# Kernel tuning notes

Hardware: AMD Instinct MI355X
Metric: run time of the kernel (lower is better)

## Reference

```python
import jax, jax.numpy as jnp
import numpy as np
from jax import lax

N = 4096      # nodes
D = 256       # in_channels
H = 128       # hidden_size (cell output = 2*H = 256)
BLOCK = 128   # row-block size for the masked-max scan
THR = 0.99    # adjacency threshold on uniform A -> avg degree ~41
EPS = 1e-12


def _block_max(m, scores):
    # m: [BLOCK, N] bool, scores: [N, H] -> [BLOCK, H]
    v = jnp.where(m[:, :, None], scores[None, :, :], -jnp.inf)
    return v.max(axis=1)

_block_max = jax.checkpoint(_block_max)


def masked_max(mask, scores):
    # maxpool over neighbors, blocked over destination nodes to avoid an [N,N,H] temp
    n = mask.shape[0]
    mblk = mask.reshape(n // BLOCK, BLOCK, n)
    def body(_, m):
        return None, _block_max(m, scores)
    _, out = lax.scan(body, None, mblk)
    out = out.reshape(n, scores.shape[-1])
    # nodes with no neighbors -> 0
    return jnp.where(jnp.isneginf(out), jnp.zeros_like(out), out)


def setup_inputs() -> dict:
    key = jax.random.key(0)
    ks = jax.random.split(key, 16)
    def w(k, shape):
        fan = shape[0]
        return (jax.random.normal(k, shape, jnp.float32) / np.sqrt(fan)).astype(jnp.float32)
    D1 = 2 * H  # layer-1 input dim (= 256)
    return dict(
        x=jax.random.normal(ks[0], (N, D), jnp.float32),
        A=jax.random.uniform(ks[1], (N, N), dtype=jnp.float32),
        # layer 0 cell params
        Wp0=w(ks[2], (D, H)), bp0=jnp.zeros((H,), jnp.float32),
        Ws0=w(ks[3], (D, H)), bs0=jnp.zeros((H,), jnp.float32),
        Wn0=w(ks[4], (H, H)), bn0=jnp.zeros((H,), jnp.float32),
        # layer 1 cell params
        Wp1=w(ks[5], (D1, H)), bp1=jnp.zeros((H,), jnp.float32),
        Ws1=w(ks[6], (D1, H)), bs1=jnp.zeros((H,), jnp.float32),
        Wn1=w(ks[7], (H, H)), bn1=jnp.zeros((H,), jnp.float32),
    )


def _cell(x, mask, Wp, bp, Ws, bs, Wn, bn):
    # GraphSAGE maxpool cell: concat(self transform, neighbor maxpool transform)
    scores = jax.nn.relu(x @ Wp + bp)                 # [N, H]
    pooled = masked_max(mask, scores)                 # [N, H]
    return jnp.concatenate([x @ Ws + bs, pooled @ Wn + bn], axis=-1)  # [N, 2H]


def reference(x, A, Wp0, bp0, Ws0, bs0, Wn0, bn0, Wp1, bp1, Ws1, bs1, Wn1, bn1):
    mask = A > THR  # [N, N] bool adjacency
    for (Wp, bp, Ws, bs, Wn, bn) in ((Wp0, bp0, Ws0, bs0, Wn0, bn0),
                                     (Wp1, bp1, Ws1, bs1, Wn1, bn1)):
        x = _cell(x, mask, Wp, bp, Ws, bs, Wn, bn)
        x = jax.nn.relu(x)
        nrm = jnp.linalg.norm(x, axis=-1, keepdims=True)
        x = x / jnp.maximum(nrm, EPS)
    return x
```

## Files before the change

kernel.cpp:

```cpp
#include <hip/hip_runtime.h>

#define NN 4096
#define CAP 256
#define THRV 0.99f

typedef __attribute__((ext_vector_type(8))) short short8v;
typedef __attribute__((ext_vector_type(4))) float f32x4;

__device__ inline unsigned short f2bf(float f) {
  unsigned u = __builtin_bit_cast(unsigned, f);
  u = (u + 0x7fffu + ((u >> 16) & 1u)) >> 16;
  return (unsigned short)u;
}
__device__ inline unsigned pkmax(unsigned a, unsigned b) {
  unsigned r;
  asm("v_pk_max_u16 %0, %1, %2" : "=v"(r) : "v"(a), "v"(b));
  return r;
}
__device__ inline uint4 max4(uint4 a, uint4 b) {
  return make_uint4(pkmax(a.x, b.x), pkmax(a.y, b.y), pkmax(a.z, b.z), pkmax(a.w, b.w));
}


__global__ __launch_bounds__(256) void kA(
    const float* __restrict__ x, const float* __restrict__ A,
    const float* __restrict__ Wp0, const float* __restrict__ bp0,
    const float* __restrict__ Ws0, const float* __restrict__ bs0,
    const float* __restrict__ Wn0, const float* __restrict__ Wp1,
    const float* __restrict__ Ws1, const float* __restrict__ Wn1,
    int* __restrict__ cnt, unsigned short* __restrict__ nbr,
    unsigned short* __restrict__ scores0, float* __restrict__ S0,
    unsigned short* __restrict__ tWn0, unsigned short* __restrict__ tWp1,
    unsigned short* __restrict__ tWs1, unsigned short* __restrict__ tWn1) {
  const int bid = blockIdx.x;
  if (bid < NN) {
    int row = bid;
    __shared__ int sc;
    __shared__ unsigned short sn[CAP];
    if (threadIdx.x == 0) sc = 0;
    __syncthreads();
    const float4* Arow = (const float4*)(A + (size_t)row * NN);
#pragma unroll
    for (int it = 0; it < 4; ++it) {
      int j4 = it * 256 + threadIdx.x;
      float4 v = Arow[j4];
      int j = j4 * 4;
      if (v.x > THRV) { int p = atomicAdd(&sc, 1); if (p < CAP) sn[p] = (unsigned short)(j); }
      if (v.y > THRV) { int p = atomicAdd(&sc, 1); if (p < CAP) sn[p] = (unsigned short)(j + 1); }
      if (v.z > THRV) { int p = atomicAdd(&sc, 1); if (p < CAP) sn[p] = (unsigned short)(j + 2); }
      if (v.w > THRV) { int p = atomicAdd(&sc, 1); if (p < CAP) sn[p] = (unsigned short)(j + 3); }
    }
    __syncthreads();
    int c = min(sc, CAP);
    if (threadIdx.x == 0) cnt[row] = c;
    for (int k = threadIdx.x; k < c; k += 256) nbr[(size_t)row * CAP + k] = sn[k];
    return;
  }
  if (bid < NN + 128) {
    const int wv = threadIdx.x >> 6, lane = threadIdx.x & 63;
    const int unit = (bid - NN) * 4 + wv;
    const int set = unit >> 8;
    const int rb = unit & 255;
    const float* W = set ? Ws0 : Wp0;
    const float* bias = set ? bs0 : bp0;
    const int g = lane >> 4, r15 = lane & 15;
    const int row = rb * 16 + r15;
    f32x4 acc[8] = {};
    for (int kt = 0; kt < 256; kt += 32) {
      const float* xp = x + (size_t)row * 256 + kt + 4 * g;
      float4 lo = *(const float4*)xp;
      float4 hi = *(const float4*)(xp + 16);
      short8v a;
      a[0] = (short)f2bf(lo.x); a[1] = (short)f2bf(lo.y);
      a[2] = (short)f2bf(lo.z); a[3] = (short)f2bf(lo.w);
      a[4] = (short)f2bf(hi.x); a[5] = (short)f2bf(hi.y);
      a[6] = (short)f2bf(hi.z); a[7] = (short)f2bf(hi.w);
#pragma unroll
      for (int nf = 0; nf < 8; ++nf) {
        const float* wp = W + (size_t)(kt + 4 * g) * 128 + nf * 16 + r15;
        short8v b;
#pragma unroll
        for (int j = 0; j < 4; ++j) b[j] = (short)f2bf(wp[(size_t)j * 128]);
#pragma unroll
        for (int j = 0; j < 4; ++j) b[4 + j] = (short)f2bf(wp[(size_t)(16 + j) * 128]);
        acc[nf] = __builtin_amdgcn_mfma_f32_16x16x32_bf16(a, b, acc[nf], 0, 0, 0);
      }
    }
#pragma unroll
    for (int nf = 0; nf < 8; ++nf) {
      int col = nf * 16 + r15;
      float bv = bias[col];
#pragma unroll
      for (int r = 0; r < 4; ++r) {
        int orow = rb * 16 + 4 * g + r;
        float t = acc[nf][r] + bv;
        if (set == 0) scores0[(size_t)orow * 128 + col] = f2bf(fmaxf(t, 0.f));
        else          S0[(size_t)orow * 128 + col] = t;
      }
    }
    return;
  }
  int id = bid - NN - 128;
  const float* src; unsigned short* dst; int base;
  if (id < 16)      { src = Wn0; dst = tWn0; base = id; }
  else if (id < 48) { src = Wp1; dst = tWp1; base = id - 16; }
  else if (id < 80) { src = Ws1; dst = tWs1; base = id - 48; }
  else              { src = Wn1; dst = tWn1; base = id - 80; }
  int e0 = base * 1024 + threadIdx.x * 4;
  float4 v = *(const float4*)(src + e0);
  int k = e0 >> 7, n = e0 & 127;
  float vv[4] = {v.x, v.y, v.z, v.w};
  int elem = (k & 3) + 4 * ((k >> 4) & 1);
  int gg = (k >> 2) & 3;
  int fragkt = (k >> 5) * 8;
#pragma unroll
  for (int i = 0; i < 4; ++i) {
    int nn = n + i;
    int idx = ((fragkt + (nn >> 4)) << 9) + ((gg * 16 + (nn & 15)) << 3) + elem;
    dst[idx] = f2bf(vv[i]);
  }
}

template<int LAYER>
__global__ __launch_bounds__(512) void fusedL(
    const int* __restrict__ cnt, const unsigned short* __restrict__ nbr,
    const unsigned short* __restrict__ scores_in, const float* __restrict__ S_in,
    const unsigned short* __restrict__ tWn, const float* __restrict__ bn,
    const unsigned short* __restrict__ tWp, const float* __restrict__ bp,
    const unsigned short* __restrict__ tWs, const float* __restrict__ bs,
    unsigned short* __restrict__ scores_out, float* __restrict__ S_out,
    float* __restrict__ out) {
  __shared__ int scnt[16];
  __shared__ unsigned short snb[16][CAP];
  __shared__ unsigned short pool2[16][2][136];
  __shared__ unsigned short pooled[16][136];
  __shared__ unsigned short xb[16][264];
  __shared__ float ssqs[16];
  __shared__ float ssqw[4][16];

  const int tid = threadIdx.x;
  const int wv = tid >> 6, lane = tid & 63, g = lane >> 4, r15 = lane & 15;
  const int r0 = blockIdx.x * 16;

  if (tid < 16) scnt[tid] = cnt[r0 + tid];
  {
    const ushort4* src = (const ushort4*)(nbr + (size_t)r0 * CAP);
    ushort4* dst = (ushort4*)snb;
    dst[tid] = src[tid];
    dst[tid + 512] = src[tid + 512];
  }
  __syncthreads();

  {
    const int r = tid >> 5, sub = tid & 31;
    const int h = sub >> 4, c8 = (sub & 15) * 8;
    const int c = scnt[r];
    uint4 m0 = make_uint4(0, 0, 0, 0), m1 = m0, m2 = m0, m3 = m0;
    int k = h;
    for (; k + 6 < c; k += 8) {
      int j0 = snb[r][k], j1 = snb[r][k + 2], j2 = snb[r][k + 4], j3 = snb[r][k + 6];
      uint4 a0 = *(const uint4*)(scores_in + (size_t)j0 * 128 + c8);
      uint4 a1 = *(const uint4*)(scores_in + (size_t)j1 * 128 + c8);
      uint4 a2 = *(const uint4*)(scores_in + (size_t)j2 * 128 + c8);
      uint4 a3 = *(const uint4*)(scores_in + (size_t)j3 * 128 + c8);
      m0 = max4(m0, a0); m1 = max4(m1, a1); m2 = max4(m2, a2); m3 = max4(m3, a3);
    }
    for (; k < c; k += 2)
      m0 = max4(m0, *(const uint4*)(scores_in + (size_t)snb[r][k] * 128 + c8));
    *(uint4*)&pool2[r][h][c8] = max4(max4(m0, m1), max4(m2, m3));
  }
  __syncthreads();
  if (tid < 256) {
    const int r = tid >> 4, c8 = (tid & 15) * 8;
    uint4 a = *(const uint4*)&pool2[r][0][c8];
    uint4 b = *(const uint4*)&pool2[r][1][c8];
    *(uint4*)&pooled[r][c8] = max4(a, b);
  }
  __syncthreads();

  float sv[8];
  f32x4 pacc[2] = {};
  const int srow = tid >> 4, sc8 = (tid & 15) * 8;
  if (tid < 256) {
    const float* sp = S_in + (size_t)(r0 + srow) * 128 + sc8;
    float4 sa = *(const float4*)sp;
    float4 sb = *(const float4*)(sp + 4);
    sv[0] = fmaxf(sa.x, 0.f); sv[1] = fmaxf(sa.y, 0.f);
    sv[2] = fmaxf(sa.z, 0.f); sv[3] = fmaxf(sa.w, 0.f);
    sv[4] = fmaxf(sb.x, 0.f); sv[5] = fmaxf(sb.y, 0.f);
    sv[6] = fmaxf(sb.z, 0.f); sv[7] = fmaxf(sb.w, 0.f);
    float ps = 0.f;
#pragma unroll
    for (int i = 0; i < 8; ++i) ps += sv[i] * sv[i];
#pragma unroll
    for (int off = 1; off < 16; off <<= 1) ps += __shfl_xor(ps, off, 16);
    if ((tid & 15) == 0) ssqs[srow] = ps;
  } else {
    const int wv2 = wv - 4;
#pragma unroll
    for (int kt = 0; kt < 128; kt += 32) {
      ushort4 alo = *(const ushort4*)&pooled[r15][kt + 4 * g];
      ushort4 ahi = *(const ushort4*)&pooled[r15][kt + 16 + 4 * g];
      short8v a;
      a[0] = alo.x; a[1] = alo.y; a[2] = alo.z; a[3] = alo.w;
      a[4] = ahi.x; a[5] = ahi.y; a[6] = ahi.z; a[7] = ahi.w;
#pragma unroll
      for (int f = 0; f < 2; ++f) {
        uint4 bw = *((const uint4*)(tWn + (size_t)((kt >> 5) * 8 + 2 * wv2 + f) * 512) + lane);
        pacc[f] = __builtin_amdgcn_mfma_f32_16x16x32_bf16(a, __builtin_bit_cast(short8v, bw), pacc[f], 0, 0, 0);
      }
    }
#pragma unroll
    for (int f = 0; f < 2; ++f) {
      float bv = bn[(2 * wv2 + f) * 16 + r15];
#pragma unroll
      for (int rr = 0; rr < 4; ++rr) pacc[f][rr] = fmaxf(pacc[f][rr] + bv, 0.f);
    }
#pragma unroll
    for (int rr = 0; rr < 4; ++rr) {
      float ps = pacc[0][rr] * pacc[0][rr] + pacc[1][rr] * pacc[1][rr];
#pragma unroll
      for (int off = 1; off < 16; off <<= 1) ps += __shfl_xor(ps, off, 16);
      if (r15 == 0) ssqw[wv2][4 * g + rr] = ps;
    }
  }
  __syncthreads();

  if (LAYER == 0) {
    if (tid < 256) {
      float tot = ssqs[srow] + ssqw[0][srow] + ssqw[1][srow] + ssqw[2][srow] + ssqw[3][srow];
      float sc = 1.f / fmaxf(sqrtf(tot), 1e-12f);
      unsigned short hh[8];
#pragma unroll
      for (int i = 0; i < 8; ++i) hh[i] = f2bf(sv[i] * sc);
      uint4 wvv;
      wvv.x = (unsigned)hh[0] | ((unsigned)hh[1] << 16);
      wvv.y = (unsigned)hh[2] | ((unsigned)hh[3] << 16);
      wvv.z = (unsigned)hh[4] | ((unsigned)hh[5] << 16);
      wvv.w = (unsigned)hh[6] | ((unsigned)hh[7] << 16);
      *(uint4*)&xb[srow][sc8] = wvv;
    } else {
      const int wv2 = wv - 4;
#pragma unroll
      for (int rr = 0; rr < 4; ++rr) {
        int row = 4 * g + rr;
        float tot = ssqs[row] + ssqw[0][row] + ssqw[1][row] + ssqw[2][row] + ssqw[3][row];
        float sc = 1.f / fmaxf(sqrtf(tot), 1e-12f);
#pragma unroll
        for (int f = 0; f < 2; ++f)
          xb[row][128 + (2 * wv2 + f) * 16 + r15] = f2bf(pacc[f][rr] * sc);
      }
    }
    __syncthreads();
    const int s = wv >> 2;
    const unsigned short* Wt = s ? tWs : tWp;
    const float* bb = s ? bs : bp;
    const int nf0 = (wv & 3) * 2;
    f32x4 dacc[2] = {};
#pragma unroll
    for (int kt = 0; kt < 256; kt += 32) {
      ushort4 alo = *(const ushort4*)&xb[r15][kt + 4 * g];
      ushort4 ahi = *(const ushort4*)&xb[r15][kt + 16 + 4 * g];
      short8v a;
      a[0] = alo.x; a[1] = alo.y; a[2] = alo.z; a[3] = alo.w;
      a[4] = ahi.x; a[5] = ahi.y; a[6] = ahi.z; a[7] = ahi.w;
#pragma unroll
      for (int f = 0; f < 2; ++f) {
        uint4 bw = *((const uint4*)(Wt + (size_t)((kt >> 5) * 8 + nf0 + f) * 512) + lane);
        dacc[f] = __builtin_amdgcn_mfma_f32_16x16x32_bf16(a, __builtin_bit_cast(short8v, bw), dacc[f], 0, 0, 0);
      }
    }
#pragma unroll
    for (int f = 0; f < 2; ++f) {
      int col = (nf0 + f) * 16 + r15;
      float bv = bb[col];
#pragma unroll
      for (int rr = 0; rr < 4; ++rr) {
        int grow = r0 + 4 * g + rr;
        float t = dacc[f][rr] + bv;
        if (s == 0) scores_out[(size_t)grow * 128 + col] = f2bf(fmaxf(t, 0.f));
        else        S_out[(size_t)grow * 128 + col] = t;
      }
    }
  } else {
    if (tid < 256) {
      float tot = ssqs[srow] + ssqw[0][srow] + ssqw[1][srow] + ssqw[2][srow] + ssqw[3][srow];
      float sc = 1.f / fmaxf(sqrtf(tot), 1e-12f);
      float* op = out + (size_t)(r0 + srow) * 256 + sc8;
      *(float4*)op = make_float4(sv[0] * sc, sv[1] * sc, sv[2] * sc, sv[3] * sc);
      *(float4*)(op + 4) = make_float4(sv[4] * sc, sv[5] * sc, sv[6] * sc, sv[7] * sc);
    } else {
      const int wv2 = wv - 4;
#pragma unroll
      for (int rr = 0; rr < 4; ++rr) {
        int row = 4 * g + rr;
        float tot = ssqs[row] + ssqw[0][row] + ssqw[1][row] + ssqw[2][row] + ssqw[3][row];
        float sc = 1.f / fmaxf(sqrtf(tot), 1e-12f);
#pragma unroll
        for (int f = 0; f < 2; ++f)
          out[(size_t)(r0 + row) * 256 + 128 + (2 * wv2 + f) * 16 + r15] = pacc[f][rr] * sc;
      }
    }
  }
}

extern "C" void kernel_launch(void* const* d_in, const int* in_sizes, int n_in,
                              void* d_out, int out_size, void* d_ws, size_t ws_size,
                              hipStream_t stream) {
  (void)in_sizes; (void)n_in; (void)out_size; (void)ws_size;
  const float* x   = (const float*)d_in[0];
  const float* A   = (const float*)d_in[1];
  const float* Wp0 = (const float*)d_in[2];
  const float* bp0 = (const float*)d_in[3];
  const float* Ws0 = (const float*)d_in[4];
  const float* bs0 = (const float*)d_in[5];
  const float* Wn0 = (const float*)d_in[6];
  const float* bn0 = (const float*)d_in[7];
  const float* Wp1 = (const float*)d_in[8];
  const float* bp1 = (const float*)d_in[9];
  const float* Ws1 = (const float*)d_in[10];
  const float* bs1 = (const float*)d_in[11];
  const float* Wn1 = (const float*)d_in[12];
  const float* bn1 = (const float*)d_in[13];

  char* ws = (char*)d_ws;
  auto alloc = [&](size_t bytes) { char* p = ws; ws += (bytes + 255) & ~(size_t)255; return p; };
  int* cnt             = (int*)alloc((size_t)NN * 4);
  unsigned short* nbr  = (unsigned short*)alloc((size_t)NN * CAP * 2);
  unsigned short* tWn0 = (unsigned short*)alloc(128 * 128 * 2);
  unsigned short* tWp1 = (unsigned short*)alloc(256 * 128 * 2);
  unsigned short* tWs1 = (unsigned short*)alloc(256 * 128 * 2);
  unsigned short* tWn1 = (unsigned short*)alloc(128 * 128 * 2);
  unsigned short* scores0 = (unsigned short*)alloc((size_t)NN * 128 * 2);
  unsigned short* scores1 = (unsigned short*)alloc((size_t)NN * 128 * 2);
  float* S0            = (float*)alloc((size_t)NN * 128 * 4);
  float* S1            = (float*)alloc((size_t)NN * 128 * 4);

  kA<<<NN + 128 + 96, 256, 0, stream>>>(x, A, Wp0, bp0, Ws0, bs0,
                                        Wn0, Wp1, Ws1, Wn1,
                                        cnt, nbr, scores0, S0,
                                        tWn0, tWp1, tWs1, tWn1);
  fusedL<0><<<NN / 16, 512, 0, stream>>>(cnt, nbr, scores0, S0,
                                         tWn0, bn0, tWp1, bp1, tWs1, bs1,
                                         scores1, S1, nullptr);
  fusedL<1><<<NN / 16, 512, 0, stream>>>(cnt, nbr, scores1, S1,
                                         tWn1, bn1, nullptr, nullptr, nullptr, nullptr,
                                         nullptr, nullptr, (float*)d_out);
}
```

Before: 55.35 us.

## Restructure adjacency scan to 8 rows per block with wave-prefix compaction

```diff
diff --git a/kernel.cpp b/kernel.cpp
--- a/kernel.cpp
+++ b/kernel.cpp
@@ -21,6 +21,10 @@
   return make_uint4(pkmax(a.x, b.x), pkmax(a.y, b.y), pkmax(a.z, b.z), pkmax(a.w, b.w));
 }
 
+
+#define GEMM_BLKS 128
+#define PREP_BLKS 96
+#define SCAN_BLKS 512
 
 __global__ __launch_bounds__(256) void kA(
     const float* __restrict__ x, const float* __restrict__ A,
@@ -33,32 +37,9 @@
     unsigned short* __restrict__ tWn0, unsigned short* __restrict__ tWp1,
     unsigned short* __restrict__ tWs1, unsigned short* __restrict__ tWn1) {
   const int bid = blockIdx.x;
-  if (bid < NN) {
-    int row = bid;
-    __shared__ int sc;
-    __shared__ unsigned short sn[CAP];
-    if (threadIdx.x == 0) sc = 0;
-    __syncthreads();
-    const float4* Arow = (const float4*)(A + (size_t)row * NN);
-#pragma unroll
-    for (int it = 0; it < 4; ++it) {
-      int j4 = it * 256 + threadIdx.x;
-      float4 v = Arow[j4];
-      int j = j4 * 4;
-      if (v.x > THRV) { int p = atomicAdd(&sc, 1); if (p < CAP) sn[p] = (unsigned short)(j); }
-      if (v.y > THRV) { int p = atomicAdd(&sc, 1); if (p < CAP) sn[p] = (unsigned short)(j + 1); }
-      if (v.z > THRV) { int p = atomicAdd(&sc, 1); if (p < CAP) sn[p] = (unsigned short)(j + 2); }
-      if (v.w > THRV) { int p = atomicAdd(&sc, 1); if (p < CAP) sn[p] = (unsigned short)(j + 3); }
-    }
-    __syncthreads();
-    int c = min(sc, CAP);
-    if (threadIdx.x == 0) cnt[row] = c;
-    for (int k = threadIdx.x; k < c; k += 256) nbr[(size_t)row * CAP + k] = sn[k];
-    return;
-  }
-  if (bid < NN + 128) {
+  if (bid < GEMM_BLKS) {
     const int wv = threadIdx.x >> 6, lane = threadIdx.x & 63;
-    const int unit = (bid - NN) * 4 + wv;
+    const int unit = bid * 4 + wv;
     const int set = unit >> 8;
     const int rb = unit & 255;
     const float* W = set ? Ws0 : Wp0;
@@ -100,24 +81,82 @@
     }
     return;
   }
-  int id = bid - NN - 128;
-  const float* src; unsigned short* dst; int base;
-  if (id < 16)      { src = Wn0; dst = tWn0; base = id; }
-  else if (id < 48) { src = Wp1; dst = tWp1; base = id - 16; }
-  else if (id < 80) { src = Ws1; dst = tWs1; base = id - 48; }
-  else              { src = Wn1; dst = tWn1; base = id - 80; }
-  int e0 = base * 1024 + threadIdx.x * 4;
-  float4 v = *(const float4*)(src + e0);
-  int k = e0 >> 7, n = e0 & 127;
-  float vv[4] = {v.x, v.y, v.z, v.w};
-  int elem = (k & 3) + 4 * ((k >> 4) & 1);
-  int gg = (k >> 2) & 3;
-  int fragkt = (k >> 5) * 8;
-#pragma unroll
-  for (int i = 0; i < 4; ++i) {
-    int nn = n + i;
-    int idx = ((fragkt + (nn >> 4)) << 9) + ((gg * 16 + (nn & 15)) << 3) + elem;
-    dst[idx] = f2bf(vv[i]);
+  if (bid < GEMM_BLKS + PREP_BLKS) {
+    int id = bid - GEMM_BLKS;
+    const float* src; unsigned short* dst; int base;
+    if (id < 16)      { src = Wn0; dst = tWn0; base = id; }
+    else if (id < 48) { src = Wp1; dst = tWp1; base = id - 16; }
+    else if (id < 80) { src = Ws1; dst = tWs1; base = id - 48; }
+    else              { src = Wn1; dst = tWn1; base = id - 80; }
+    int e0 = base * 1024 + threadIdx.x * 4;
+    float4 v = *(const float4*)(src + e0);
+    int k = e0 >> 7, n = e0 & 127;
+    float vv[4] = {v.x, v.y, v.z, v.w};
+    int elem = (k & 3) + 4 * ((k >> 4) & 1);
+    int gg = (k >> 2) & 3;
+    int fragkt = (k >> 5) * 8;
+#pragma unroll
+    for (int i = 0; i < 4; ++i) {
+      int nn = n + i;
+      int idx = ((fragkt + (nn >> 4)) << 9) + ((gg * 16 + (nn & 15)) << 3) + elem;
+      dst[idx] = f2bf(vv[i]);
+    }
+    return;
+  }
+  {
+    __shared__ int scnt[8];
+    __shared__ unsigned short snb[8][CAP];
+    const int t = threadIdx.x;
+    const int lane = t & 63;
+    const int r0 = (bid - GEMM_BLKS - PREP_BLKS) * 8;
+    if (t < 8) scnt[t] = 0;
+    __syncthreads();
+    const float4* base = (const float4*)(A + (size_t)r0 * NN) + 4 * t;
+    float4 c0 = base[0], c1 = base[1], c2 = base[2], c3 = base[3];
+    for (int r = 0; r < 8; ++r) {
+      float4 n0 = c0, n1 = c1, n2 = c2, n3 = c3;
+      if (r < 7) {
+        const float4* nb = base + (size_t)(r + 1) * (NN / 4);
+        n0 = nb[0]; n1 = nb[1]; n2 = nb[2]; n3 = nb[3];
+      }
+      unsigned m = 0;
+      m |= (c0.x > THRV) ? 0x1u : 0u;    m |= (c0.y > THRV) ? 0x2u : 0u;
+      m |= (c0.z > THRV) ? 0x4u : 0u;    m |= (c0.w > THRV) ? 0x8u : 0u;
+      m |= (c1.x > THRV) ? 0x10u : 0u;   m |= (c1.y > THRV) ? 0x20u : 0u;
+      m |= (c1.z > THRV) ? 0x40u : 0u;   m |= (c1.w > THRV) ? 0x80u : 0u;
+      m |= (c2.x > THRV) ? 0x100u : 0u;  m |= (c2.y > THRV) ? 0x200u : 0u;
+      m |= (c2.z > THRV) ? 0x400u : 0u;  m |= (c2.w > THRV) ? 0x800u : 0u;
+      m |= (c3.x > THRV) ? 0x1000u : 0u; m |= (c3.y > THRV) ? 0x2000u : 0u;
+      m |= (c3.z > THRV) ? 0x4000u : 0u; m |= (c3.w > THRV) ? 0x8000u : 0u;
+      int cntT = __popc(m);
+      int inc = cntT;
+#pragma unroll
+      for (int off = 1; off < 64; off <<= 1) {
+        int o = __shfl_up(inc, off, 64);
+        if (lane >= off) inc += o;
+      }
+      int excl = inc - cntT;
+      int wtot = __shfl(inc, 63, 64);
+      int wbase = 0;
+      if (lane == 0) wbase = atomicAdd(&scnt[r], wtot);
+      wbase = __shfl(wbase, 0, 64);
+      int pos = wbase + excl;
+      while (m) {
+        int i = __ffs(m) - 1;
+        m &= m - 1;
+        if (pos < CAP) snb[r][pos] = (unsigned short)(16 * t + i);
+        ++pos;
+      }
+      c0 = n0; c1 = n1; c2 = n2; c3 = n3;
+    }
+    __syncthreads();
+    if (t < 8) cnt[r0 + t] = min(scnt[t], CAP);
+    {
+      ushort4* dst = (ushort4*)(nbr + (size_t)r0 * CAP);
+      const ushort4* s = (const ushort4*)snb;
+      dst[t] = s[t];
+      dst[t + 256] = s[t + 256];
+    }
   }
 }
 
@@ -336,10 +375,9 @@
   float* S0            = (float*)alloc((size_t)NN * 128 * 4);
   float* S1            = (float*)alloc((size_t)NN * 128 * 4);
 
-  kA<<<NN + 128 + 96, 256, 0, stream>>>(x, A, Wp0, bp0, Ws0, bs0,
-                                        Wn0, Wp1, Ws1, Wn1,
-                                        cnt, nbr, scores0, S0,
-                                        tWn0, tWp1, tWs1, tWn1);
+  kA<<<GEMM_BLKS + PREP_BLKS + SCAN_BLKS, 256, 0, stream>>>(
+      x, A, Wp0, bp0, Ws0, bs0, Wn0, Wp1, Ws1, Wn1,
+      cnt, nbr, scores0, S0, tWn0, tWp1, tWs1, tWn1);
   fusedL<0><<<NN / 16, 512, 0, stream>>>(cnt, nbr, scores0, S0,
                                          tWn0, bn0, tWp1, bp1, tWs1, bs1,
                                          scores1, S1, nullptr);
```

Result: faster. 51.60 us (-6.8%).
